# Kernel optimization log

Measured on AMD Instinct MI355X. Metric: run time of the kernel, lower is better.

The kernel has to match this reference:

```python
import jax, jax.numpy as jnp
import numpy as np

N, E = 50000, 800000
IN, HID, OUT = 128, 256, 128
BN_EPS = 1e-5


def setup_inputs() -> dict:
    key = jax.random.key(0)
    ks = jax.random.split(key, 12)
    x = jax.random.normal(ks[0], (N, IN), dtype=jnp.float32)
    edge_index = jax.random.randint(ks[1], (2, E), 0, N, dtype=jnp.int64)
    edge_weight = jax.random.uniform(ks[2], (E,), dtype=jnp.float32)
    # GCNConv weights (glorot-ish scale) and biases
    W0 = jax.random.normal(ks[3], (IN, HID), dtype=jnp.float32) * (1.0 / np.sqrt(IN))
    b0 = jnp.zeros((HID,), jnp.float32)
    W1 = jax.random.normal(ks[4], (HID, HID), dtype=jnp.float32) * (1.0 / np.sqrt(HID))
    b1 = jnp.zeros((HID,), jnp.float32)
    Wl = jax.random.normal(ks[5], (HID, OUT), dtype=jnp.float32) * (1.0 / np.sqrt(HID))
    bl = jnp.zeros((OUT,), jnp.float32)
    # BatchNorm affine params (eval mode: running_mean=0, running_var=1)
    g0 = 1.0 + 0.1 * jax.random.normal(ks[6], (HID,), dtype=jnp.float32)
    be0 = 0.1 * jax.random.normal(ks[7], (HID,), dtype=jnp.float32)
    g1 = 1.0 + 0.1 * jax.random.normal(ks[8], (HID,), dtype=jnp.float32)
    be1 = 0.1 * jax.random.normal(ks[9], (HID,), dtype=jnp.float32)
    return {"x": x, "edge_index": edge_index, "edge_weight": edge_weight,
            "W0": W0, "b0": b0, "W1": W1, "b1": b1, "Wl": Wl, "bl": bl,
            "g0": g0, "be0": be0, "g1": g1, "be1": be1}


def reference(x, edge_index, edge_weight, W0, b0, W1, b1, Wl, bl, g0, be0, g1, be1):
    n = x.shape[0]
    row, col = edge_index[0], edge_index[1]
    # add self-loops with weight 1 (GCNConv default)
    ar = jnp.arange(n)
    rowf = jnp.concatenate([row, ar])
    colf = jnp.concatenate([col, ar])
    wf = jnp.concatenate([edge_weight, jnp.ones((n,), x.dtype)])
    # symmetric normalization: D^{-1/2} A D^{-1/2}
    deg = jax.ops.segment_sum(wf, colf, num_segments=n)
    dinv = jnp.where(deg > 0, jax.lax.rsqrt(deg), 0.0)
    norm = dinv[rowf] * wf * dinv[colf]  # [E+N]

    def conv(h, W, b):
        h = h @ W                       # [n, d_out]
        msg = h[rowf] * norm[:, None]   # gather + scale per edge
        return jax.ops.segment_sum(msg, colf, num_segments=n) + b

    def bn_eval(h, g, b):
        # eval-mode BN with running_mean=0, running_var=1
        return h * (g / jnp.sqrt(1.0 + BN_EPS)) + b

    h = jax.nn.relu(bn_eval(conv(x, W0, b0), g0, be0))
    h = jax.nn.relu(bn_eval(conv(h, W1, b1), g1, be1))
    h = conv(h, Wl, bl)
    return jax.nn.log_softmax(h, axis=1)
```

## Files before the change

### kernel.cpp

```cpp
#include <hip/hip_runtime.h>
#include <cstddef>
#include <cstdint>


#define GCN_BN_EPS 1e-5f
#define NB_CHUNK 256

typedef short v8bf __attribute__((ext_vector_type(8)));
typedef float v4f __attribute__((ext_vector_type(4)));


__device__ __forceinline__ float4 unpack_bf4(uint2 u) {
  float4 r;
  r.x = __uint_as_float(u.x << 16);
  r.y = __uint_as_float(u.x & 0xffff0000u);
  r.z = __uint_as_float(u.y << 16);
  r.w = __uint_as_float(u.y & 0xffff0000u);
  return r;
}
__device__ __forceinline__ uint16_t f2bf(float f) {
  uint32_t u = __float_as_uint(f);
  return (uint16_t)((u + 0x7fffu + ((u >> 16) & 1u)) >> 16);
}
__device__ __forceinline__ uint2 pack_bf4(float4 v) {
  uint2 r;
  r.x = (uint32_t)f2bf(v.x) | ((uint32_t)f2bf(v.y) << 16);
  r.y = (uint32_t)f2bf(v.z) | ((uint32_t)f2bf(v.w) << 16);
  return r;
}
__device__ __forceinline__ float f16tof(unsigned int hi16) {
  return (float)__builtin_bit_cast(_Float16, (unsigned short)hi16);
}


__global__ __launch_bounds__(256) void build_hist_kernel(
    const int* __restrict__ ei, const float* __restrict__ ew,
    int* __restrict__ col_, uint2* __restrict__ pk,
    unsigned int* __restrict__ histw, float* __restrict__ degw, int E, int n) {
  extern __shared__ unsigned int h8[];
  __shared__ int s_flag;
  const int b = blockIdx.x;
  const int nw = (n + 3) >> 2;
  if (threadIdx.x == 0) {
    int nz = 0;
    for (int k = 1; k < 64; k += 2) nz |= ei[k];
    s_flag = (nz == 0) ? 1 : 0;
  }
  for (int i = threadIdx.x; i < nw; i += 256) h8[i] = 0u;
  __syncthreads();
  const int flag = s_flag;
  const int per = (E + NB_CHUNK - 1) / NB_CHUNK;
  const int e0 = b * per, e1 = min(e0 + per, E);
  for (int e = e0 + threadIdx.x; e < e1; e += 256) {
    int r, c;
    if (flag) { r = ei[2 * e]; c = ei[2 * (E + e)]; }
    else      { r = ei[e];     c = ei[E + e]; }
    float w = ew[e];
    col_[e] = c;
    pk[e] = make_uint2((unsigned)r, __float_as_uint(w));
    atomicAdd(&h8[c >> 2], 1u << ((c & 3) * 8));
    atomicAdd(&degw[c], w);
  }
  __syncthreads();
  for (int i = threadIdx.x; i < nw; i += 256)
    histw[(size_t)b * nw + i] = h8[i];
}

__global__ __launch_bounds__(256) void scan1_conv_kernel(
    const unsigned int* __restrict__ histw, unsigned int* __restrict__ cntw,
    int* __restrict__ bsum, int nw, int nB,
    const float* __restrict__ x, uint16_t* __restrict__ xb,
    const float* __restrict__ W0, uint16_t* __restrict__ W0t,
    const float* __restrict__ W1, uint16_t* __restrict__ W1t,
    const float* __restrict__ Wl, uint16_t* __restrict__ Wlt,
    const float* __restrict__ degw, float* __restrict__ dinv,
    int t0, int convTot) {
  if (blockIdx.x >= nB) {
    int i = (blockIdx.x - nB) * 256 + threadIdx.x;
    if (i >= convTot) return;
    if (i < t0) {
      float4 v = *(const float4*)&x[(size_t)i * 4];
      *(uint2*)&xb[(size_t)i * 4] = pack_bf4(v);
      return;
    }
    int j = i - t0;
    if (j < 128 * 256) { int nn = j >> 7, k = j & 127; W0t[j] = f2bf(W0[(size_t)k * 256 + nn]); return; }
    j -= 128 * 256;
    if (j < 256 * 256) { int nn = j >> 8, k = j & 255; W1t[j] = f2bf(W1[(size_t)k * 256 + nn]); return; }
    j -= 256 * 256;
    if (j < 256 * 128) { int nn = j >> 8, k = j & 255; Wlt[j] = f2bf(Wl[(size_t)k * 128 + nn]); return; }
    j -= 256 * 128;
    dinv[j] = rsqrtf(1.0f + degw[j]);
    return;
  }
  __shared__ int ws[4];
  const int j = blockIdx.x * 256 + threadIdx.x;
  unsigned int acc = 0;
  if (j < nw)
    for (int b = 0; b < NB_CHUNK; ++b) acc += histw[(size_t)b * nw + j];
  if (j < nw) cntw[j] = acc;
  int s = (int)((acc & 0xffu) + ((acc >> 8) & 0xffu) + ((acc >> 16) & 0xffu) + (acc >> 24));
  int x_ = s;
#pragma unroll
  for (int st = 1; st < 64; st <<= 1) x_ += __shfl_xor(x_, st, 64);
  if ((threadIdx.x & 63) == 0) ws[threadIdx.x >> 6] = x_;
  __syncthreads();
  if (threadIdx.x == 0) bsum[blockIdx.x] = ws[0] + ws[1] + ws[2] + ws[3];
}

__global__ __launch_bounds__(256) void scan3_base_kernel(
    const unsigned int* __restrict__ cntw, const int* __restrict__ bsum,
    int* __restrict__ off, unsigned int* __restrict__ histw,
    int nw, int nB, int n, int E) {
  __shared__ int wsum[4], woff[4];
  __shared__ int s_gbase;
  const int tid = threadIdx.x, lane = tid & 63, wv = tid >> 6;
  const int j = blockIdx.x * 256 + tid;
  unsigned int cw = (j < nw) ? cntw[j] : 0u;
  const int c0 = (int)(cw & 0xffu), c1 = (int)((cw >> 8) & 0xffu);
  const int c2 = (int)((cw >> 16) & 0xffu), c3 = (int)(cw >> 24);
  int s = c0 + c1 + c2 + c3;
  int x = s;
#pragma unroll
  for (int st = 1; st < 64; st <<= 1) { int t = __shfl_up(x, st, 64); if (lane >= st) x += t; }
  if (lane == 63) wsum[wv] = x;
  __syncthreads();
  if (tid == 0) { int r = 0; for (int k = 0; k < 4; ++k) { woff[k] = r; r += wsum[k]; } }
  if (wv == 0) {
    int v2 = (lane < nB) ? bsum[lane] : 0;
    int y = v2;
#pragma unroll
    for (int st = 1; st < 64; st <<= 1) { int t = __shfl_up(y, st, 64); if (lane >= st) y += t; }
    if (lane == blockIdx.x) s_gbase = y - v2;
  }
  __syncthreads();
  if (j < nw) {
    int excl = x - s + woff[wv] + s_gbase;
    uint4 o4;
    o4.x = excl; o4.y = excl + c0; o4.z = excl + c0 + c1; o4.w = excl + c0 + c1 + c2;
    *(uint4*)&off[4 * j] = o4;
    unsigned int run = 0;
    for (int b = 0; b < NB_CHUNK; ++b) {
      size_t idx = (size_t)b * nw + j;
      unsigned int w = histw[idx];
      histw[idx] = run;
      run += w;
    }
  }
  if (blockIdx.x == 0 && tid == 0) off[n] = E;
}

__global__ __launch_bounds__(256) void fill_kernel(
    const int* __restrict__ col_, const uint2* __restrict__ pk,
    const int* __restrict__ off, const unsigned int* __restrict__ histw,
    const float* __restrict__ dinv, unsigned int* __restrict__ csr4,
    int E, int n) {
  extern __shared__ unsigned int c8[];
  const int b = blockIdx.x;
  const int nw = (n + 3) >> 2;
  for (int i = threadIdx.x; i < nw; i += 256) c8[i] = 0u;
  __syncthreads();
  const int per = (E + NB_CHUNK - 1) / NB_CHUNK;
  const int e0 = b * per, e1 = min(e0 + per, E);
  const unsigned int* brel = histw + (size_t)b * nw;
  for (int e = e0 + threadIdx.x; e < e1; e += 256) {
    int c = col_[e];
    const int sh = (c & 3) * 8;
    unsigned old = atomicAdd(&c8[c >> 2], 1u << sh);
    int rel = (int)((old >> sh) & 0xffu) + (int)((brel[c >> 2] >> sh) & 0xffu);
    uint2 v = pk[e];
    float nv = dinv[(int)v.x] * __uint_as_float(v.y);
    unsigned short hb = __builtin_bit_cast(unsigned short, (_Float16)nv);
    csr4[off[c] + rel] = (v.x & 0xffffu) | ((unsigned int)hb << 16);
  }
}


template <int EPI>
__global__ __launch_bounds__(256) void agg256_kernel(
    const uint16_t* __restrict__ hin, uint16_t* __restrict__ hout,
    const int* __restrict__ off, const unsigned int* __restrict__ csr4,
    const float* __restrict__ dinv,
    const float* __restrict__ bias, const float* __restrict__ g,
    const float* __restrict__ be, int n) {
  const int lane = threadIdx.x & 63;
  const int c = blockIdx.x * 4 + (threadIdx.x >> 6);
  if (c >= n) return;
  const int f = lane * 4;
  const int e0 = off[c], e1 = off[c + 1];
  const float di = dinv[c];
  float4 self = unpack_bf4(*(const uint2*)&hin[(size_t)c * 256 + f]);
  float4 acc = make_float4(self.x * di, self.y * di, self.z * di, self.w * di);

  for (int base = e0; base < e1; base += 64) {
    int idx = base + lane;
    unsigned int ev = (idx < e1) ? __builtin_nontemporal_load(&csr4[idx]) : 0u;
    const int m = min(64, e1 - base);
    const int nG = (m + 3) >> 2;
    for (int gI = 0; gI < nG; ++gI) {
      int e_ = gI * 4;
      unsigned int ea = __shfl(ev, e_, 64);
      unsigned int eb = __shfl(ev, e_ + 1, 64);
      unsigned int ec = __shfl(ev, e_ + 2, 64);
      unsigned int ed = __shfl(ev, e_ + 3, 64);
      float v0 = f16tof(ea >> 16), v1 = f16tof(eb >> 16);
      float v2 = f16tof(ec >> 16), v3 = f16tof(ed >> 16);
      float4 h0 = unpack_bf4(*(const uint2*)&hin[(size_t)(ea & 0xffffu) * 256 + f]);
      float4 h1 = unpack_bf4(*(const uint2*)&hin[(size_t)(eb & 0xffffu) * 256 + f]);
      float4 h2 = unpack_bf4(*(const uint2*)&hin[(size_t)(ec & 0xffffu) * 256 + f]);
      float4 h3 = unpack_bf4(*(const uint2*)&hin[(size_t)(ed & 0xffffu) * 256 + f]);
      acc.x += v0 * h0.x + v1 * h1.x + v2 * h2.x + v3 * h3.x;
      acc.y += v0 * h0.y + v1 * h1.y + v2 * h2.y + v3 * h3.y;
      acc.z += v0 * h0.z + v1 * h1.z + v2 * h2.z + v3 * h3.z;
      acc.w += v0 * h0.w + v1 * h1.w + v2 * h2.w + v3 * h3.w;
    }
  }

  acc.x *= di; acc.y *= di; acc.z *= di; acc.w *= di;
  if (EPI == 1) {
    const float bns = rsqrtf(1.0f + GCN_BN_EPS);
    float4 bi = *(const float4*)&bias[f];
    float4 gi = *(const float4*)&g[f];
    float4 bei = *(const float4*)&be[f];
    acc.x = fmaxf((acc.x + bi.x) * gi.x * bns + bei.x, 0.0f);
    acc.y = fmaxf((acc.y + bi.y) * gi.y * bns + bei.y, 0.0f);
    acc.z = fmaxf((acc.z + bi.z) * gi.z * bns + bei.z, 0.0f);
    acc.w = fmaxf((acc.w + bi.w) * gi.w * bns + bei.w, 0.0f);
  }
  *(uint2*)&hout[(size_t)c * 256 + f] = pack_bf4(acc);
}

template <int EPI>
__global__ __launch_bounds__(256) void agg128_kernel(
    const uint16_t* __restrict__ hin, void* __restrict__ hout_,
    const int* __restrict__ off, const unsigned int* __restrict__ csr4,
    const float* __restrict__ dinv, const float* __restrict__ bias, int n) {
  const int lane = threadIdx.x & 63;
  const int sub = lane & 31;
  const int hbase = lane & 32;
  const int c = blockIdx.x * 8 + (threadIdx.x >> 6) * 2 + (lane >> 5);
  const bool active = (c < n);
  const int f = sub * 4;

  int e0 = 0, e1 = 0;
  float di = 0.0f;
  float4 acc = make_float4(0.f, 0.f, 0.f, 0.f);
  if (active) {
    e0 = off[c]; e1 = off[c + 1];
    di = dinv[c];
    float4 self = unpack_bf4(*(const uint2*)&hin[(size_t)c * 128 + f]);
    acc = make_float4(self.x * di, self.y * di, self.z * di, self.w * di);
  }
  int nch = (e1 - e0 + 31) >> 5;
  nch = max(nch, __shfl(nch, lane ^ 32));

  for (int ch = 0; ch < nch; ++ch) {
    int idx = e0 + ch * 32 + sub;
    unsigned int ev = 0u;
    if (active && idx < e1) ev = __builtin_nontemporal_load(&csr4[idx]);
    int m = e1 - (e0 + ch * 32);
    m = m < 0 ? 0 : (m > 32 ? 32 : m);
    int mMax = max(m, __shfl(m, lane ^ 32));
    const int nG = (mMax + 3) >> 2;
    for (int gI = 0; gI < nG; ++gI) {
      int e_ = hbase + gI * 4;
      unsigned int ea = __shfl(ev, e_, 64);
      unsigned int eb = __shfl(ev, e_ + 1, 64);
      unsigned int ec = __shfl(ev, e_ + 2, 64);
      unsigned int ed = __shfl(ev, e_ + 3, 64);
      int s0 = (int)(ea & 0xffffu); float v0 = f16tof(ea >> 16);
      int s1 = (int)(eb & 0xffffu); float v1 = f16tof(eb >> 16);
      int sB = (int)(ec & 0xffffu); float v2 = f16tof(ec >> 16);
      int s3 = (int)(ed & 0xffffu); float v3 = f16tof(ed >> 16);
      float4 h0 = unpack_bf4(*(const uint2*)&hin[(size_t)s0 * 128 + f]);
      float4 h1 = unpack_bf4(*(const uint2*)&hin[(size_t)s1 * 128 + f]);
      float4 h2 = unpack_bf4(*(const uint2*)&hin[(size_t)sB * 128 + f]);
      float4 h3 = unpack_bf4(*(const uint2*)&hin[(size_t)s3 * 128 + f]);
      acc.x += v0 * h0.x + v1 * h1.x + v2 * h2.x + v3 * h3.x;
      acc.y += v0 * h0.y + v1 * h1.y + v2 * h2.y + v3 * h3.y;
      acc.z += v0 * h0.z + v1 * h1.z + v2 * h2.z + v3 * h3.z;
      acc.w += v0 * h0.w + v1 * h1.w + v2 * h2.w + v3 * h3.w;
    }
  }

  acc.x *= di; acc.y *= di; acc.z *= di; acc.w *= di;
  if (EPI == 0) {
    uint16_t* hout = (uint16_t*)hout_;
    if (active) *(uint2*)&hout[(size_t)c * 128 + f] = pack_bf4(acc);
  } else {
    float* hout = (float*)hout_;
    float4 bi = active ? *(const float4*)&bias[f] : make_float4(0.f, 0.f, 0.f, 0.f);
    float tx = acc.x + bi.x, ty = acc.y + bi.y, tz = acc.z + bi.z, tw = acc.w + bi.w;
    float mx = fmaxf(fmaxf(tx, ty), fmaxf(tz, tw));
#pragma unroll
    for (int s = 1; s < 32; s <<= 1) mx = fmaxf(mx, __shfl_xor(mx, s, 64));
    float ex = expf(tx - mx) + expf(ty - mx) + expf(tz - mx) + expf(tw - mx);
#pragma unroll
    for (int s = 1; s < 32; s <<= 1) ex += __shfl_xor(ex, s, 64);
    float lse = logf(ex) + mx;
    if (active) {
      float4 res = make_float4(tx - lse, ty - lse, tz - lse, tw - lse);
      *(float4*)&hout[(size_t)c * 128 + f] = res;
    }
  }
}

template <int K, int NC, int EPI>
__global__ __launch_bounds__(256) void mfma_gemm_kernel(
    const uint16_t* __restrict__ A, const uint16_t* __restrict__ WT,
    uint16_t* __restrict__ Cb, int M, int tpb,
    const float* __restrict__ bias, const float* __restrict__ g,
    const float* __restrict__ be) {
  constexpr int CW = NC / 4;
  constexpr int NT = CW / 16;
  constexpr int KS = K / 32;
  const int lane = threadIdx.x & 63;
  const int wave = threadIdx.x >> 6;
  const int quad = lane >> 4;
  const int l16 = lane & 15;
  const int col0 = wave * CW;

  const int tiles = (M + 15) >> 4;
  int t0 = blockIdx.x * tpb;
  if (t0 >= tiles) return;
  int t1 = min(t0 + tpb, tiles);

  v8bf b[KS][NT];
#pragma unroll
  for (int ks = 0; ks < KS; ++ks)
#pragma unroll
    for (int nt = 0; nt < NT; ++nt)
      b[ks][nt] = *(const v8bf*)(WT + (size_t)(col0 + nt * 16 + l16) * K +
                                 ks * 32 + quad * 8);

  float sc[NT], o1[NT], o2[NT];
  if (EPI == 1) {
    const float bns = rsqrtf(1.0f + GCN_BN_EPS);
#pragma unroll
    for (int nt = 0; nt < NT; ++nt) {
      int col = col0 + nt * 16 + l16;
      sc[nt] = g[col] * bns; o1[nt] = bias[col]; o2[nt] = be[col];
    }
  }

  v8bf a[KS], an[KS];
  {
    int arow = min(t0 * 16 + l16, M - 1);
    const uint16_t* Ap = A + (size_t)arow * K + quad * 8;
#pragma unroll
    for (int ks = 0; ks < KS; ++ks) a[ks] = *(const v8bf*)(Ap + ks * 32);
  }
  for (int t = t0; t < t1; ++t) {
    if (t + 1 < t1) {
      int arow = min((t + 1) * 16 + l16, M - 1);
      const uint16_t* Ap = A + (size_t)arow * K + quad * 8;
#pragma unroll
      for (int ks = 0; ks < KS; ++ks) an[ks] = *(const v8bf*)(Ap + ks * 32);
    }
    v4f acc[NT];
#pragma unroll
    for (int nt = 0; nt < NT; ++nt) acc[nt] = (v4f){0.f, 0.f, 0.f, 0.f};
#pragma unroll
    for (int ks = 0; ks < KS; ++ks)
#pragma unroll
      for (int nt = 0; nt < NT; ++nt)
        acc[nt] = __builtin_amdgcn_mfma_f32_16x16x32_bf16(a[ks], b[ks][nt],
                                                          acc[nt], 0, 0, 0);
    const int row0 = t * 16 + quad * 4;
#pragma unroll
    for (int nt = 0; nt < NT; ++nt) {
      const int col = col0 + nt * 16 + l16;
#pragma unroll
      for (int r = 0; r < 4; ++r) {
        int row = row0 + r;
        if (row < M) {
          float v = acc[nt][r];
          if (EPI == 1) v = fmaxf((v + o1[nt]) * sc[nt] + o2[nt], 0.0f);
          Cb[(size_t)row * NC + col] = f2bf(v);
        }
      }
    }
#pragma unroll
    for (int ks = 0; ks < KS; ++ks) a[ks] = an[ks];
  }
}


static inline char* carve(char*& p, size_t bytes) {
  char* r = p;
  p += (bytes + 255) & ~(size_t)255;
  return r;
}

extern "C" void kernel_launch(void* const* d_in, const int* in_sizes, int n_in,
                              void* d_out, int out_size, void* d_ws, size_t ws_size,
                              hipStream_t stream) {
  const int N = in_sizes[0] / 128;
  const int E = in_sizes[2];

  const float* x  = (const float*)d_in[0];
  const int*   ei = (const int*)d_in[1];
  const float* ew = (const float*)d_in[2];
  const float* W0 = (const float*)d_in[3];
  const float* b0 = (const float*)d_in[4];
  const float* W1 = (const float*)d_in[5];
  const float* b1 = (const float*)d_in[6];
  const float* Wl = (const float*)d_in[7];
  const float* bl = (const float*)d_in[8];
  const float* g0 = (const float*)d_in[9];
  const float* be0 = (const float*)d_in[10];
  const float* g1 = (const float*)d_in[11];
  const float* be1 = (const float*)d_in[12];
  float* out = (float*)d_out;

  const int nw = (N + 3) / 4;

  char* p = (char*)d_ws;
  float*        dinv  = (float*)carve(p, (size_t)N * 4);
  float*        degw  = (float*)carve(p, (size_t)N * 4);
  unsigned int* cntw  = (unsigned int*)carve(p, (size_t)nw * 4);
  int*          off   = (int*)carve(p, (size_t)(N + 1) * 4);
  int*          bsum  = (int*)carve(p, 1024 * 4);
  int*          col_  = (int*)carve(p, (size_t)E * 4);
  uint2*        pk    = (uint2*)carve(p, (size_t)E * 8);
  unsigned int* csr4  = (unsigned int*)carve(p, (size_t)E * 4);
  unsigned int* histw = (unsigned int*)carve(p, (size_t)NB_CHUNK * nw * 4);
  uint16_t*     xb16  = (uint16_t*)carve(p, (size_t)N * 128 * 2);
  uint16_t*     bufR  = (uint16_t*)carve(p, (size_t)N * 128 * 2);
  uint16_t*     bufP  = (uint16_t*)carve(p, (size_t)N * 256 * 2);
  uint16_t*     bufQ  = (uint16_t*)carve(p, (size_t)N * 256 * 2);
  uint16_t*     W0t   = (uint16_t*)carve(p, (size_t)128 * 256 * 2);
  uint16_t*     W1t   = (uint16_t*)carve(p, (size_t)256 * 256 * 2);
  uint16_t*     Wlt   = (uint16_t*)carve(p, (size_t)256 * 128 * 2);

  const int TB = 256;
  const int gW4 = (N + 3) / 4;
  const int gW8 = (N + 7) / 8;
  const int tiles = (N + 15) / 16;
  const int TPB = 8;
  const int gG = (tiles + TPB - 1) / TPB;
  const size_t ldsU8 = (size_t)nw * 4;
  const int nB = (nw + 255) / 256;
  const int convT0 = N * 32;
  const int convTot = convT0 + 128 * 256 + 256 * 256 + 256 * 128 + N;
  const int convB = (convTot + TB - 1) / TB;

  hipMemsetAsync(degw, 0, (size_t)N * 4, stream);
  build_hist_kernel<<<NB_CHUNK, TB, ldsU8, stream>>>(ei, ew, col_, pk, histw,
                                                     degw, E, N);
  scan1_conv_kernel<<<nB + convB, TB, 0, stream>>>(histw, cntw, bsum, nw, nB,
                                                   x, xb16, W0, W0t, W1, W1t,
                                                   Wl, Wlt, degw, dinv,
                                                   convT0, convTot);
  scan3_base_kernel<<<nB, TB, 0, stream>>>(cntw, bsum, off, histw, nw, nB, N, E);
  fill_kernel<<<NB_CHUNK, TB, ldsU8, stream>>>(col_, pk, off, histw, dinv,
                                               csr4, E, N);

  agg128_kernel<0><<<gW8, 256, 0, stream>>>(xb16, bufR, off, csr4, dinv,
                                            nullptr, N);
  mfma_gemm_kernel<128, 256, 1><<<gG, 256, 0, stream>>>(bufR, W0t, bufP, N, TPB,
                                                        b0, g0, be0);
  mfma_gemm_kernel<256, 256, 0><<<gG, 256, 0, stream>>>(bufP, W1t, bufQ, N, TPB,
                                                        nullptr, nullptr, nullptr);
  agg256_kernel<1><<<gW4, 256, 0, stream>>>(bufQ, bufP, off, csr4, dinv,
                                            b1, g1, be1, N);
  mfma_gemm_kernel<256, 128, 0><<<gG, 256, 0, stream>>>(bufP, Wlt, bufR, N, TPB,
                                                        nullptr, nullptr, nullptr);
  agg128_kernel<2><<<gW8, 256, 0, stream>>>(bufR, out, off, csr4, dinv, bl, N);
}
```

Measured before the change: 385.6 us.

## Split aggregation by feature chunk with XCD-affine work queues; drop degree atomics

```diff
diff --git a/kernel.cpp b/kernel.cpp
--- a/kernel.cpp
+++ b/kernel.cpp
@@ -36,7 +36,7 @@
 __global__ __launch_bounds__(256) void build_hist_kernel(
     const int* __restrict__ ei, const float* __restrict__ ew,
     int* __restrict__ col_, uint2* __restrict__ pk,
-    unsigned int* __restrict__ histw, float* __restrict__ degw, int E, int n) {
+    unsigned int* __restrict__ histw, int E, int n) {
   extern __shared__ unsigned int h8[];
   __shared__ int s_flag;
   const int b = blockIdx.x;
@@ -55,11 +55,9 @@
     int r, c;
     if (flag) { r = ei[2 * e]; c = ei[2 * (E + e)]; }
     else      { r = ei[e];     c = ei[E + e]; }
-    float w = ew[e];
     col_[e] = c;
-    pk[e] = make_uint2((unsigned)r, __float_as_uint(w));
+    pk[e] = make_uint2((unsigned)r, __float_as_uint(ew[e]));
     atomicAdd(&h8[c >> 2], 1u << ((c & 3) * 8));
-    atomicAdd(&degw[c], w);
   }
   __syncthreads();
   for (int i = threadIdx.x; i < nw; i += 256)
@@ -73,7 +71,6 @@
     const float* __restrict__ W0, uint16_t* __restrict__ W0t,
     const float* __restrict__ W1, uint16_t* __restrict__ W1t,
     const float* __restrict__ Wl, uint16_t* __restrict__ Wlt,
-    const float* __restrict__ degw, float* __restrict__ dinv,
     int t0, int convTot) {
   if (blockIdx.x >= nB) {
     int i = (blockIdx.x - nB) * 256 + threadIdx.x;
@@ -88,9 +85,7 @@
     j -= 128 * 256;
     if (j < 256 * 256) { int nn = j >> 8, k = j & 255; W1t[j] = f2bf(W1[(size_t)k * 256 + nn]); return; }
     j -= 256 * 256;
-    if (j < 256 * 128) { int nn = j >> 8, k = j & 255; Wlt[j] = f2bf(Wl[(size_t)k * 128 + nn]); return; }
-    j -= 256 * 128;
-    dinv[j] = rsqrtf(1.0f + degw[j]);
+    if (j < 256 * 128) { int nn = j >> 8, k = j & 255; Wlt[j] = f2bf(Wl[(size_t)k * 128 + nn]); }
     return;
   }
   __shared__ int ws[4];
@@ -153,8 +148,7 @@
 __global__ __launch_bounds__(256) void fill_kernel(
     const int* __restrict__ col_, const uint2* __restrict__ pk,
     const int* __restrict__ off, const unsigned int* __restrict__ histw,
-    const float* __restrict__ dinv, unsigned int* __restrict__ csr4,
-    int E, int n) {
+    uint2* __restrict__ csr, int E, int n) {
   extern __shared__ unsigned int c8[];
   const int b = blockIdx.x;
   const int nw = (n + 3) >> 2;
@@ -168,66 +162,107 @@
     const int sh = (c & 3) * 8;
     unsigned old = atomicAdd(&c8[c >> 2], 1u << sh);
     int rel = (int)((old >> sh) & 0xffu) + (int)((brel[c >> 2] >> sh) & 0xffu);
-    uint2 v = pk[e];
-    float nv = dinv[(int)v.x] * __uint_as_float(v.y);
-    unsigned short hb = __builtin_bit_cast(unsigned short, (_Float16)nv);
-    csr4[off[c] + rel] = (v.x & 0xffffu) | ((unsigned int)hb << 16);
-  }
-}
-
-
-template <int EPI>
-__global__ __launch_bounds__(256) void agg256_kernel(
+    csr[off[c] + rel] = pk[e];
+  }
+}
+
+__global__ void degdinv_kernel(const int* __restrict__ off, const uint2* __restrict__ csr,
+                               float* __restrict__ dinv, int n) {
+  int i = blockIdx.x * blockDim.x + threadIdx.x;
+  if (i >= n) return;
+  float s = 1.0f;
+  int p1 = off[i + 1];
+  for (int p = off[i]; p < p1; ++p) s += __uint_as_float(csr[p].y);
+  dinv[i] = rsqrtf(s);
+}
+
+__global__ __launch_bounds__(256) void csr4conv_kernel(
+    const uint2* __restrict__ csr, const float* __restrict__ dinv,
+    unsigned int* __restrict__ csr4, int E) {
+  int e = blockIdx.x * 256 + threadIdx.x;
+  if (e >= E) return;
+  uint2 v = csr[e];
+  float nv = dinv[(int)v.x] * __uint_as_float(v.y);
+  unsigned short hb = __builtin_bit_cast(unsigned short, (_Float16)nv);
+  csr4[e] = (v.x & 0xffffu) | ((unsigned int)hb << 16);
+}
+
+template <int D, int EPI>
+__global__ __launch_bounds__(256) void aggx_kernel(
     const uint16_t* __restrict__ hin, uint16_t* __restrict__ hout,
     const int* __restrict__ off, const unsigned int* __restrict__ csr4,
-    const float* __restrict__ dinv,
-    const float* __restrict__ bias, const float* __restrict__ g,
-    const float* __restrict__ be, int n) {
+    const float* __restrict__ dinv, const float* __restrict__ bias,
+    const float* __restrict__ g, const float* __restrict__ be,
+    int* __restrict__ q, int n) {
+  constexpr int NCH = D / 32;
   const int lane = threadIdx.x & 63;
-  const int c = blockIdx.x * 4 + (threadIdx.x >> 6);
-  if (c >= n) return;
-  const int f = lane * 4;
-  const int e0 = off[c], e1 = off[c + 1];
-  const float di = dinv[c];
-  float4 self = unpack_bf4(*(const uint2*)&hin[(size_t)c * 256 + f]);
-  float4 acc = make_float4(self.x * di, self.y * di, self.z * di, self.w * di);
-
-  for (int base = e0; base < e1; base += 64) {
-    int idx = base + lane;
-    unsigned int ev = (idx < e1) ? __builtin_nontemporal_load(&csr4[idx]) : 0u;
-    const int m = min(64, e1 - base);
-    const int nG = (m + 3) >> 2;
-    for (int gI = 0; gI < nG; ++gI) {
-      int e_ = gI * 4;
-      unsigned int ea = __shfl(ev, e_, 64);
-      unsigned int eb = __shfl(ev, e_ + 1, 64);
-      unsigned int ec = __shfl(ev, e_ + 2, 64);
-      unsigned int ed = __shfl(ev, e_ + 3, 64);
-      float v0 = f16tof(ea >> 16), v1 = f16tof(eb >> 16);
-      float v2 = f16tof(ec >> 16), v3 = f16tof(ed >> 16);
-      float4 h0 = unpack_bf4(*(const uint2*)&hin[(size_t)(ea & 0xffffu) * 256 + f]);
-      float4 h1 = unpack_bf4(*(const uint2*)&hin[(size_t)(eb & 0xffffu) * 256 + f]);
-      float4 h2 = unpack_bf4(*(const uint2*)&hin[(size_t)(ec & 0xffffu) * 256 + f]);
-      float4 h3 = unpack_bf4(*(const uint2*)&hin[(size_t)(ed & 0xffffu) * 256 + f]);
-      acc.x += v0 * h0.x + v1 * h1.x + v2 * h2.x + v3 * h3.x;
-      acc.y += v0 * h0.y + v1 * h1.y + v2 * h2.y + v3 * h3.y;
-      acc.z += v0 * h0.z + v1 * h1.z + v2 * h2.z + v3 * h3.z;
-      acc.w += v0 * h0.w + v1 * h1.w + v2 * h2.w + v3 * h3.w;
-    }
-  }
-
-  acc.x *= di; acc.y *= di; acc.z *= di; acc.w *= di;
-  if (EPI == 1) {
-    const float bns = rsqrtf(1.0f + GCN_BN_EPS);
-    float4 bi = *(const float4*)&bias[f];
-    float4 gi = *(const float4*)&g[f];
-    float4 bei = *(const float4*)&be[f];
-    acc.x = fmaxf((acc.x + bi.x) * gi.x * bns + bei.x, 0.0f);
-    acc.y = fmaxf((acc.y + bi.y) * gi.y * bns + bei.y, 0.0f);
-    acc.z = fmaxf((acc.z + bi.z) * gi.z * bns + bei.z, 0.0f);
-    acc.w = fmaxf((acc.w + bi.w) * gi.w * bns + bei.w, 0.0f);
-  }
-  *(uint2*)&hout[(size_t)c * 256 + f] = pack_bf4(acc);
+  const int ls = lane & 7;
+  const int sb = lane & ~7;
+  const int niw = lane >> 3;
+  const int ngroups = (n + 31) >> 5;
+  unsigned xcd;
+  asm volatile("s_getreg_b32 %0, hwreg(HW_REG_XCC_ID)" : "=s"(xcd));
+  const int pref = (int)xcd & (NCH - 1);
+  const float bns = rsqrtf(1.0f + GCN_BN_EPS);
+
+  for (int t = 0; t < NCH; ++t) {
+    const int ch = (pref + t) & (NCH - 1);
+    const int fo = ch * 32 + ls * 4;
+    while (true) {
+      int gid;
+      if (lane == 0) {
+        int snap = __hip_atomic_load(&q[ch * 32], __ATOMIC_RELAXED,
+                                     __HIP_MEMORY_SCOPE_AGENT);
+        gid = (snap < ngroups) ? atomicAdd(&q[ch * 32], 1) : ngroups;
+      }
+      gid = __shfl(gid, 0, 64);
+      if (gid >= ngroups) break;
+      const int cb = gid * 32;
+#pragma unroll
+      for (int s4 = 0; s4 < 4; ++s4) {
+        const int c = cb + s4 * 8 + niw;
+        if (c >= n) continue;
+        const int e0 = off[c], e1 = off[c + 1];
+        const float di = dinv[c];
+        float4 acc = unpack_bf4(*(const uint2*)&hin[(size_t)c * D + fo]);
+        acc.x *= di; acc.y *= di; acc.z *= di; acc.w *= di;
+        for (int base = e0; base < e1; base += 8) {
+          int idx = base + ls;
+          unsigned int ev = (idx < e1) ? __builtin_nontemporal_load(&csr4[idx]) : 0u;
+          const int m = min(8, e1 - base);
+          const int nG = (m + 3) >> 2;
+          for (int gI = 0; gI < nG; ++gI) {
+            int e_ = sb + gI * 4;
+            unsigned int ea = __shfl(ev, e_, 64);
+            unsigned int eb = __shfl(ev, e_ + 1, 64);
+            unsigned int ec = __shfl(ev, e_ + 2, 64);
+            unsigned int ed = __shfl(ev, e_ + 3, 64);
+            float v0 = f16tof(ea >> 16), v1 = f16tof(eb >> 16);
+            float v2 = f16tof(ec >> 16), v3 = f16tof(ed >> 16);
+            float4 h0 = unpack_bf4(*(const uint2*)&hin[(size_t)(ea & 0xffffu) * D + fo]);
+            float4 h1 = unpack_bf4(*(const uint2*)&hin[(size_t)(eb & 0xffffu) * D + fo]);
+            float4 h2 = unpack_bf4(*(const uint2*)&hin[(size_t)(ec & 0xffffu) * D + fo]);
+            float4 h3 = unpack_bf4(*(const uint2*)&hin[(size_t)(ed & 0xffffu) * D + fo]);
+            acc.x += v0 * h0.x + v1 * h1.x + v2 * h2.x + v3 * h3.x;
+            acc.y += v0 * h0.y + v1 * h1.y + v2 * h2.y + v3 * h3.y;
+            acc.z += v0 * h0.z + v1 * h1.z + v2 * h2.z + v3 * h3.z;
+            acc.w += v0 * h0.w + v1 * h1.w + v2 * h2.w + v3 * h3.w;
+          }
+        }
+        acc.x *= di; acc.y *= di; acc.z *= di; acc.w *= di;
+        if (EPI == 1) {
+          float4 bi = *(const float4*)&bias[fo];
+          float4 gi = *(const float4*)&g[fo];
+          float4 bei = *(const float4*)&be[fo];
+          acc.x = fmaxf((acc.x + bi.x) * gi.x * bns + bei.x, 0.0f);
+          acc.y = fmaxf((acc.y + bi.y) * gi.y * bns + bei.y, 0.0f);
+          acc.z = fmaxf((acc.z + bi.z) * gi.z * bns + bei.z, 0.0f);
+          acc.w = fmaxf((acc.w + bi.w) * gi.w * bns + bei.w, 0.0f);
+        }
+        *(uint2*)&hout[(size_t)c * D + fo] = pack_bf4(acc);
+      }
+    }
+  }
 }
 
 template <int EPI>
@@ -417,13 +452,13 @@
 
   char* p = (char*)d_ws;
   float*        dinv  = (float*)carve(p, (size_t)N * 4);
-  float*        degw  = (float*)carve(p, (size_t)N * 4);
   unsigned int* cntw  = (unsigned int*)carve(p, (size_t)nw * 4);
   int*          off   = (int*)carve(p, (size_t)(N + 1) * 4);
   int*          bsum  = (int*)carve(p, 1024 * 4);
+  int*          qcnt  = (int*)carve(p, 16 * 32 * 4);
   int*          col_  = (int*)carve(p, (size_t)E * 4);
   uint2*        pk    = (uint2*)carve(p, (size_t)E * 8);
-  unsigned int* csr4  = (unsigned int*)carve(p, (size_t)E * 4);
+  uint2*        csr   = (uint2*)carve(p, (size_t)E * 8);
   unsigned int* histw = (unsigned int*)carve(p, (size_t)NB_CHUNK * nw * 4);
   uint16_t*     xb16  = (uint16_t*)carve(p, (size_t)N * 128 * 2);
   uint16_t*     bufR  = (uint16_t*)carve(p, (size_t)N * 128 * 2);
@@ -432,38 +467,40 @@
   uint16_t*     W0t   = (uint16_t*)carve(p, (size_t)128 * 256 * 2);
   uint16_t*     W1t   = (uint16_t*)carve(p, (size_t)256 * 256 * 2);
   uint16_t*     Wlt   = (uint16_t*)carve(p, (size_t)256 * 128 * 2);
+  unsigned int* csr4  = (unsigned int*)col_;
 
   const int TB = 256;
-  const int gW4 = (N + 3) / 4;
+  const int gN = (N + TB - 1) / TB;
   const int gW8 = (N + 7) / 8;
+  const int gE = (E + TB - 1) / TB;
+  const int AGG_BLOCKS = 1024;
   const int tiles = (N + 15) / 16;
   const int TPB = 8;
   const int gG = (tiles + TPB - 1) / TPB;
   const size_t ldsU8 = (size_t)nw * 4;
   const int nB = (nw + 255) / 256;
   const int convT0 = N * 32;
-  const int convTot = convT0 + 128 * 256 + 256 * 256 + 256 * 128 + N;
+  const int convTot = convT0 + 128 * 256 + 256 * 256 + 256 * 128;
   const int convB = (convTot + TB - 1) / TB;
 
-  hipMemsetAsync(degw, 0, (size_t)N * 4, stream);
-  build_hist_kernel<<<NB_CHUNK, TB, ldsU8, stream>>>(ei, ew, col_, pk, histw,
-                                                     degw, E, N);
+  hipMemsetAsync(qcnt, 0, 16 * 32 * 4, stream);
+  build_hist_kernel<<<NB_CHUNK, TB, ldsU8, stream>>>(ei, ew, col_, pk, histw, E, N);
   scan1_conv_kernel<<<nB + convB, TB, 0, stream>>>(histw, cntw, bsum, nw, nB,
                                                    x, xb16, W0, W0t, W1, W1t,
-                                                   Wl, Wlt, degw, dinv,
-                                                   convT0, convTot);
+                                                   Wl, Wlt, convT0, convTot);
   scan3_base_kernel<<<nB, TB, 0, stream>>>(cntw, bsum, off, histw, nw, nB, N, E);
-  fill_kernel<<<NB_CHUNK, TB, ldsU8, stream>>>(col_, pk, off, histw, dinv,
-                                               csr4, E, N);
-
-  agg128_kernel<0><<<gW8, 256, 0, stream>>>(xb16, bufR, off, csr4, dinv,
-                                            nullptr, N);
+  fill_kernel<<<NB_CHUNK, TB, ldsU8, stream>>>(col_, pk, off, histw, csr, E, N);
+  degdinv_kernel<<<gN, TB, 0, stream>>>(off, csr, dinv, N);
+  csr4conv_kernel<<<gE, TB, 0, stream>>>(csr, dinv, csr4, E);
+
+  aggx_kernel<128, 0><<<AGG_BLOCKS, 256, 0, stream>>>(
+      xb16, bufR, off, csr4, dinv, nullptr, nullptr, nullptr, qcnt, N);
   mfma_gemm_kernel<128, 256, 1><<<gG, 256, 0, stream>>>(bufR, W0t, bufP, N, TPB,
                                                         b0, g0, be0);
   mfma_gemm_kernel<256, 256, 0><<<gG, 256, 0, stream>>>(bufP, W1t, bufQ, N, TPB,
                                                         nullptr, nullptr, nullptr);
-  agg256_kernel<1><<<gW4, 256, 0, stream>>>(bufQ, bufP, off, csr4, dinv,
-                                            b1, g1, be1, N);
+  aggx_kernel<256, 1><<<AGG_BLOCKS, 256, 0, stream>>>(
+      bufQ, bufP, off, csr4, dinv, b1, g1, be1, qcnt + 8 * 32, N);
   mfma_gemm_kernel<256, 128, 0><<<gG, 256, 0, stream>>>(bufP, Wlt, bufR, N, TPB,
                                                         nullptr, nullptr, nullptr);
   agg128_kernel<2><<<gW8, 256, 0, stream>>>(bufR, out, off, csr4, dinv, bl, N);
```

After: 587.2 us. 1.52x slower.
